# Performance work log

Measured on AMD Instinct MI355X. Metric: run time of the kernel, lower is better.

The kernel has to match this reference:

```python
import jax, jax.numpy as jnp
import numpy as np

NU, NI, E = 50000, 20000, 400000
IN, HID, OUT = 128, 256, 128
NEG_SLOPE_ATTN = 0.2   # DGL GATConv default
NEG_SLOPE_ACT = 0.01   # F.leaky_relu default
BN_EPS = 1e-5


def setup_inputs() -> dict:
    key = jax.random.key(0)
    ks = jax.random.split(key, 32)
    d = {}
    d["x_user"] = jax.random.normal(ks[0], (NU, IN), jnp.float32)
    d["x_item"] = jax.random.normal(ks[1], (NI, IN), jnp.float32)
    d["eu"] = jax.random.randint(ks[2], (E,), 0, NU, jnp.int32)
    d["ei"] = jax.random.randint(ks[3], (E,), 0, NI, jnp.int32)
    i = 4
    dims = [(IN, 4, 64), (HID, 4, 64), (HID, 4, 64), (HID, 4, 32)]
    for L, (fin, H, dh) in enumerate(dims):
        for rel in ("ui", "iu"):
            d[f"W{L}_{rel}"] = jax.random.normal(ks[i], (fin, H * dh), jnp.float32) * 0.1; i += 1
            d[f"A{L}_{rel}"] = jax.random.normal(ks[i], (2, H, dh), jnp.float32) * 0.1; i += 1
    # BN params: [layer, (gamma,beta), HID]; gamma near 1, beta near 0
    gu = 1.0 + 0.05 * jax.random.normal(ks[i], (3, 1, HID), jnp.float32); i += 1
    bu = 0.05 * jax.random.normal(ks[i], (3, 1, HID), jnp.float32); i += 1
    gi = 1.0 + 0.05 * jax.random.normal(ks[i], (3, 1, HID), jnp.float32); i += 1
    bi = 0.05 * jax.random.normal(ks[i], (3, 1, HID), jnp.float32); i += 1
    d["bn_u"] = jnp.concatenate([gu, bu], axis=1)
    d["bn_i"] = jnp.concatenate([gi, bi], axis=1)
    return d


def _gat(x_src, x_dst, W, A, src, dst, n_dst):
    # Single-relation bipartite GATConv (DGL semantics).
    H, dh = A.shape[1], A.shape[2]
    hs = (x_src @ W).reshape(-1, H, dh)           # [Ns,H,dh]
    hd = (x_dst @ W).reshape(-1, H, dh)           # [Nd,H,dh]
    el = jnp.einsum('nhd,hd->nh', hs, A[0])
    er = jnp.einsum('nhd,hd->nh', hd, A[1])
    e = jax.nn.leaky_relu(el[src] + er[dst], NEG_SLOPE_ATTN)   # [E,H]
    emax = jax.ops.segment_max(e, dst, num_segments=n_dst)
    ee = jnp.exp(e - emax[dst])
    denom = jax.ops.segment_sum(ee, dst, num_segments=n_dst)
    alpha = ee / denom[dst]                       # segment softmax over in-edges
    out = jax.ops.segment_sum(hs[src] * alpha[..., None], dst, num_segments=n_dst)
    return out.reshape(n_dst, H * dh)


def _bn(x, gamma, beta):
    mu = x.mean(axis=0)
    var = x.var(axis=0)   # biased, matches torch BN normalization
    return gamma * (x - mu) * jax.lax.rsqrt(var + BN_EPS) + beta


def reference(x_user, x_item, eu, ei, W0_ui, W0_iu, A0_ui, A0_iu,
              W1_ui, W1_iu, A1_ui, A1_iu, W2_ui, W2_iu, A2_ui, A2_iu,
              W3_ui, W3_iu, A3_ui, A3_iu, bn_u, bn_i):
    Wui = [W0_ui, W1_ui, W2_ui]; Aui = [A0_ui, A1_ui, A2_ui]
    Wiu = [W0_iu, W1_iu, W2_iu]; Aiu = [A0_iu, A1_iu, A2_iu]
    hu, hi = x_user, x_item
    for L in range(3):
        ni = _gat(hu, hi, Wui[L], Aui[L], eu, ei, NI)   # user -> item
        nu = _gat(hi, hu, Wiu[L], Aiu[L], ei, eu, NU)   # item -> user
        nu = _bn(nu, bn_u[L, 0], bn_u[L, 1])
        ni = _bn(ni, bn_i[L, 0], bn_i[L, 1])
        if L == 2:   # last hidden layer uses tanh in non-residual path
            hu, hi = jnp.tanh(nu), jnp.tanh(ni)
        else:
            hu = jax.nn.leaky_relu(nu, NEG_SLOPE_ACT)
            hi = jax.nn.leaky_relu(ni, NEG_SLOPE_ACT)
    out_i = _gat(hu, hi, W3_ui, A3_ui, eu, ei, NI)
    out_u = _gat(hi, hu, W3_iu, A3_iu, ei, eu, NU)
    return jnp.concatenate([out_u, out_i], axis=0)   # [NU+NI, OUT]
```

## Files before the change

kernel.cpp:

```cpp
#include <hip/hip_runtime.h>

#define NUSERS 50000
#define NITEMS 20000
#define NEDGES 400000

typedef _Float16 f16;
typedef __attribute__((ext_vector_type(8))) _Float16 f16x8;
typedef __attribute__((ext_vector_type(4))) _Float16 f16x4;
typedef __attribute__((ext_vector_type(2))) _Float16 f16x2;
typedef __attribute__((ext_vector_type(4))) float f32x4;

__global__ void prep_k(const float* __restrict__ Wa, const float* __restrict__ Aa,
                       f16* __restrict__ Bta, float* __restrict__ efa,
                       const float* __restrict__ Wb, const float* __restrict__ Ab,
                       f16* __restrict__ Btb, float* __restrict__ efb,
                       int K, int Nw, int dh) {
  int t = blockIdx.x * blockDim.x + threadIdx.x;
  int half = K * Nw;
  if (t >= 2 * half) return;
  const float* W = (t < half) ? Wa : Wb;
  const float* A = (t < half) ? Aa : Ab;
  f16* Bt = (t < half) ? Bta : Btb;
  float* ef = (t < half) ? efa : efb;
  int t2 = (t < half) ? t : t - half;
  int n = t2 / K, k = t2 - n * K;
  Bt[t2] = (f16)W[(long)k * Nw + n];
  if (t2 < K * 8) {
    int j = t2 / (K * 4);
    int r = t2 - j * K * 4;
    int h = r / K, f = r - h * K;
    const float* Aj = A + j * Nw;
    float s = 0.f;
    for (int d = 0; d < dh; ++d) s += W[f * Nw + h * dh + d] * Aj[h * dh + d];
    ef[j * 4 * K + h * K + f] = s;
  }
}

__global__ void xcvt_k(const float* __restrict__ xu, f16* __restrict__ yu, long nu,
                       const float* __restrict__ xi, f16* __restrict__ yi, long ni) {
  long i = (long)blockIdx.x * blockDim.x + threadIdx.x;
  if (i < nu) yu[i] = (f16)xu[i];
  else if (i < nu + ni) yi[i - nu] = (f16)xi[i - nu];
}

__global__ __launch_bounds__(256) void hgemm2_k(const f16* __restrict__ Aa, const f16* __restrict__ Bta,
                                                f16* __restrict__ Ca, int Ma, int gya,
                                                const f16* __restrict__ Ab, const f16* __restrict__ Btb,
                                                f16* __restrict__ Cb, int Mb,
                                                int N, int K) {
  __shared__ f16 As[128 * 32];
  __shared__ f16 Bs[128 * 32];
  int by = blockIdx.y;
  const f16* A; const f16* Bt; f16* C; int M; int row0;
  if (by < gya) { A = Aa; Bt = Bta; C = Ca; M = Ma; row0 = by * 128; }
  else          { A = Ab; Bt = Btb; C = Cb; M = Mb; row0 = (by - gya) * 128; }
  int tid = threadIdx.x;
  int col0 = blockIdx.x * 128;
  int lane = tid & 63, wv = tid >> 6;
  int wr = (wv & 1) * 64, wc = (wv >> 1) * 64;
  int l16 = lane & 15, q = lane >> 4;
  f32x4 acc[4][4] = {};
  int r = tid >> 2, c8 = (tid & 3) * 8;
  for (int k0 = 0; k0 < K; k0 += 32) {
    int ra = min(row0 + r, M - 1);
    uint4 va = *(const uint4*)&A[(long)ra * K + k0 + c8];
    int ra2 = min(row0 + r + 64, M - 1);
    uint4 va2 = *(const uint4*)&A[(long)ra2 * K + k0 + c8];
    uint4 vb = *(const uint4*)&Bt[(long)(col0 + r) * K + k0 + c8];
    uint4 vb2 = *(const uint4*)&Bt[(long)(col0 + r + 64) * K + k0 + c8];
    *(uint4*)&As[r * 32 + c8] = va;
    *(uint4*)&As[(r + 64) * 32 + c8] = va2;
    *(uint4*)&Bs[r * 32 + c8] = vb;
    *(uint4*)&Bs[(r + 64) * 32 + c8] = vb2;
    __syncthreads();
    f16x8 af[4], bfr[4];
#pragma unroll
    for (int i = 0; i < 4; ++i) {
      af[i] = *(const f16x8*)&As[(wr + i * 16 + l16) * 32 + q * 8];
      bfr[i] = *(const f16x8*)&Bs[(wc + i * 16 + l16) * 32 + q * 8];
    }
#pragma unroll
    for (int i = 0; i < 4; ++i)
#pragma unroll
      for (int j = 0; j < 4; ++j)
        acc[i][j] = __builtin_amdgcn_mfma_f32_16x16x32_f16(af[i], bfr[j], acc[i][j], 0, 0, 0);
    __syncthreads();
  }
#pragma unroll
  for (int i = 0; i < 4; ++i) {
#pragma unroll
    for (int reg = 0; reg < 4; ++reg) {
      int rr = row0 + wr + i * 16 + q * 4 + reg;
      if (rr < M) {
#pragma unroll
        for (int j = 0; j < 4; ++j)
          C[(long)rr * N + col0 + wc + j * 16 + l16] = (f16)acc[i][j][reg];
      }
    }
  }
}

__global__ __launch_bounds__(256) void eler_k(
    const f16* __restrict__ hbu, const float* __restrict__ ef_ui, const float* __restrict__ ef_iu,
    float* __restrict__ el_u, float* __restrict__ er_u,
    const f16* __restrict__ hbi, float* __restrict__ el_i, float* __restrict__ er_i, int K) {
  __shared__ float xs[256];
  int b = blockIdx.x, t = threadIdx.x;
  const f16* hb; const float* elf; const float* erf; float* el; float* er; int n;
  if (b < NUSERS) { hb = hbu; elf = ef_ui; erf = ef_iu + 4 * K; el = el_u; er = er_u; n = b; }
  else            { hb = hbi; elf = ef_iu; erf = ef_ui + 4 * K; el = el_i; er = er_i; n = b - NUSERS; }
  if (t < K) xs[t] = (float)hb[(long)n * K + t];
  __syncthreads();
  int j = t >> 5, l = t & 31;
  const float* fr = (j < 4) ? (elf + j * K) : (erf + (j - 4) * K);
  float p = 0.f;
  for (int f = l; f < K; f += 32) p += xs[f] * fr[f];
#pragma unroll
  for (int off = 16; off; off >>= 1) p += __shfl_down(p, off, 32);
  if (l == 0) { if (j < 4) el[n * 4 + j] = p; else er[n * 4 + (j - 4)] = p; }
}

__global__ void hist_k(const int* __restrict__ ei, int* __restrict__ degi,
                       const int* __restrict__ eu, int* __restrict__ degu) {
  int e = blockIdx.x * blockDim.x + threadIdx.x;
  if (e < NEDGES) atomicAdd(&degi[ei[e]], 1);
  else if (e < 2 * NEDGES) atomicAdd(&degu[eu[e - NEDGES]], 1);
}

__global__ __launch_bounds__(256) void scan1_k(const int* __restrict__ deg,
                                               int* __restrict__ bsum, int N) {
  __shared__ int red[256];
  int base = blockIdx.x * 1024, t = threadIdx.x;
  int s = 0;
#pragma unroll
  for (int j = 0; j < 4; ++j) { int i = base + t * 4 + j; s += (i < N) ? deg[i] : 0; }
  red[t] = s; __syncthreads();
  for (int off = 128; off; off >>= 1) { if (t < off) red[t] += red[t + off]; __syncthreads(); }
  if (t == 0) bsum[blockIdx.x] = red[0];
}

__global__ void scan2_k(int* __restrict__ bsum, int nb) {
  if (threadIdx.x == 0) {
    int run = 0;
    for (int i = 0; i < nb; ++i) { int v = bsum[i]; bsum[i] = run; run += v; }
  }
}

__global__ __launch_bounds__(256) void scan3_k(const int* __restrict__ deg,
                                               const int* __restrict__ bsum,
                                               int* __restrict__ rowptr, int N) {
  __shared__ int tsum[256];
  int base = blockIdx.x * 1024, t = threadIdx.x;
  int v[4]; int s = 0;
#pragma unroll
  for (int j = 0; j < 4; ++j) { int i = base + t * 4 + j; v[j] = (i < N) ? deg[i] : 0; s += v[j]; }
  tsum[t] = s; __syncthreads();
  for (int off = 1; off < 256; off <<= 1) {
    int x = (t >= off) ? tsum[t - off] : 0;
    __syncthreads();
    tsum[t] += x;
    __syncthreads();
  }
  int run = bsum[blockIdx.x] + ((t > 0) ? tsum[t - 1] : 0);
#pragma unroll
  for (int j = 0; j < 4; ++j) {
    int i = base + t * 4 + j;
    if (i < N) rowptr[i] = run;
    run += v[j];
  }
}

__global__ void setval_k(int* __restrict__ p, int v) { *p = v; }

__global__ void copy2_k(const int* __restrict__ a, int* __restrict__ b, int Na,
                        const int* __restrict__ c, int* __restrict__ d, int Nc) {
  int i = blockIdx.x * blockDim.x + threadIdx.x;
  if (i < Na) b[i] = a[i];
  else if (i < Na + Nc) d[i - Na] = c[i - Na];
}

__global__ void scat_k(const int* __restrict__ ei, const int* __restrict__ eu,
                       int* __restrict__ curi, int* __restrict__ srci,
                       int* __restrict__ curu, int* __restrict__ srcu) {
  int e = blockIdx.x * blockDim.x + threadIdx.x;
  if (e < NEDGES) {
    int p = atomicAdd(&curi[ei[e]], 1);
    srci[p] = eu[e];
  } else if (e < 2 * NEDGES) {
    int e2 = e - NEDGES;
    int p = atomicAdd(&curu[eu[e2]], 1);
    srcu[p] = ei[e2];
  }
}

template <int W, int DH, typename OUT>
__global__ __launch_bounds__(256) void agg_k(
    const float* __restrict__ elA, const float* __restrict__ erA,
    const int* __restrict__ rpA, const int* __restrict__ srcA,
    const f16* __restrict__ hsA, OUT* __restrict__ outA, int nA,
    const float* __restrict__ elB, const float* __restrict__ erB,
    const int* __restrict__ rpB, const int* __restrict__ srcB,
    const f16* __restrict__ hsB, OUT* __restrict__ outB, int nB) {
  constexpr int CPL = W >> 6;
  constexpr int SHIFT = (W == 256) ? 9 : 8;
  constexpr bool OF16 = (sizeof(OUT) == 2);
  __shared__ float alds[4][256];
  __shared__ int soff[4][64];
  int wv = threadIdx.x >> 6;
  int g = blockIdx.x * 4 + wv;
  int lane = threadIdx.x & 63;
  const float* el; const float* er; const int* rp; const int* srcv;
  const f16* hs; OUT* outp; int d;
  if (g < nA)           { el = elA; er = erA; rp = rpA; srcv = srcA; hs = hsA; outp = outA; d = g; }
  else if (g < nA + nB) { el = elB; er = erB; rp = rpB; srcv = srcB; hs = hsB; outp = outB; d = g - nA; }
  else return;
  int s0 = rp[d], s1 = rp[d + 1];
  int deg = s1 - s0;
  int c0 = lane * CPL;
  int h = c0 / DH;
  long obase = (long)d * W + c0;
  if (deg == 0) {
#pragma unroll
    for (int q = 0; q < CPL; ++q) outp[obase + q] = (OUT)0.f;
    return;
  }
  const float NEG = -3.0e38f;
  float acc[CPL];
#pragma unroll
  for (int q = 0; q < CPL; ++q) acc[q] = 0.f;
  float inv;

  if (deg <= 64) {
    int hh = lane & 3, p = lane >> 2;
    float er_h = er[d * 4 + hh];
    float vv[4];
    float vmax = NEG;
#pragma unroll
    for (int j = 0; j < 4; ++j) {
      int slot = j * 16 + p;
      vv[j] = NEG;
      if (slot < deg) {
        int sj = srcv[s0 + slot];
        if (hh == 0) soff[wv][slot] = sj << SHIFT;
        float v = el[sj * 4 + hh] + er_h;
        v = v > 0.f ? v : 0.2f * v;
        vv[j] = v;
        vmax = fmaxf(vmax, v);
      }
    }
#pragma unroll
    for (int off = 4; off < 64; off <<= 1) vmax = fmaxf(vmax, __shfl_xor(vmax, off, 64));
    float ssum = 0.f;
#pragma unroll
    for (int j = 0; j < 4; ++j) {
      int slot = j * 16 + p;
      if (slot < deg) {
        float e = expf(vv[j] - vmax);
        alds[wv][slot * 4 + hh] = e;
        ssum += e;
      } else {
        alds[wv][slot * 4 + hh] = 0.f;
        if (hh == 0) soff[wv][slot] = 0;
      }
    }
#pragma unroll
    for (int off = 4; off < 64; off <<= 1) ssum += __shfl_xor(ssum, off, 64);
    float Sh = __shfl(ssum, (lane & ~3) | h, 64);
    inv = 1.0f / Sh;
    const char* hbase = (const char*)hs + (size_t)c0 * sizeof(f16);
    int degp = (deg + 3) & ~3;
    for (int j = 0; j < degp; j += 4) {
      float aj[4]; int oj[4];
#pragma unroll
      for (int u = 0; u < 4; ++u) {
        aj[u] = alds[wv][(j + u) * 4 + h];
        oj[u] = soff[wv][j + u];
      }
      if constexpr (CPL == 4) {
        f16x4 vj[4];
#pragma unroll
        for (int u = 0; u < 4; ++u)
          vj[u] = *(const f16x4*)(hbase + (size_t)(unsigned)oj[u]);
#pragma unroll
        for (int u = 0; u < 4; ++u) {
          acc[0] += aj[u] * (float)vj[u][0];
          acc[1] += aj[u] * (float)vj[u][1];
          acc[2] += aj[u] * (float)vj[u][2];
          acc[3] += aj[u] * (float)vj[u][3];
        }
      } else {
        f16x2 vj[4];
#pragma unroll
        for (int u = 0; u < 4; ++u)
          vj[u] = *(const f16x2*)(hbase + (size_t)(unsigned)oj[u]);
#pragma unroll
        for (int u = 0; u < 4; ++u) {
          acc[0] += aj[u] * (float)vj[u][0];
          acc[1] += aj[u] * (float)vj[u][1];
        }
      }
    }
  } else {
    float4 er4 = *(const float4*)&er[d * 4];
    float m0 = NEG, m1 = NEG, m2 = NEG, m3 = NEG;
    for (int k = s0 + lane; k < s1; k += 64) {
      int s = srcv[k];
      float4 e4 = *(const float4*)&el[s * 4];
      float v;
      v = e4.x + er4.x; v = v > 0.f ? v : 0.2f * v; m0 = fmaxf(m0, v);
      v = e4.y + er4.y; v = v > 0.f ? v : 0.2f * v; m1 = fmaxf(m1, v);
      v = e4.z + er4.z; v = v > 0.f ? v : 0.2f * v; m2 = fmaxf(m2, v);
      v = e4.w + er4.w; v = v > 0.f ? v : 0.2f * v; m3 = fmaxf(m3, v);
    }
#pragma unroll
    for (int off = 32; off; off >>= 1) {
      m0 = fmaxf(m0, __shfl_xor(m0, off, 64));
      m1 = fmaxf(m1, __shfl_xor(m1, off, 64));
      m2 = fmaxf(m2, __shfl_xor(m2, off, 64));
      m3 = fmaxf(m3, __shfl_xor(m3, off, 64));
    }
    float S0 = 0.f, S1 = 0.f, S2 = 0.f, S3 = 0.f;
    for (int k = s0 + lane; k < s1; k += 64) {
      int s = srcv[k];
      float4 e4 = *(const float4*)&el[s * 4];
      float v;
      v = e4.x + er4.x; v = v > 0.f ? v : 0.2f * v; S0 += expf(v - m0);
      v = e4.y + er4.y; v = v > 0.f ? v : 0.2f * v; S1 += expf(v - m1);
      v = e4.z + er4.z; v = v > 0.f ? v : 0.2f * v; S2 += expf(v - m2);
      v = e4.w + er4.w; v = v > 0.f ? v : 0.2f * v; S3 += expf(v - m3);
    }
#pragma unroll
    for (int off = 32; off; off >>= 1) {
      S0 += __shfl_xor(S0, off, 64);
      S1 += __shfl_xor(S1, off, 64);
      S2 += __shfl_xor(S2, off, 64);
      S3 += __shfl_xor(S3, off, 64);
    }
    float mh = h == 0 ? m0 : h == 1 ? m1 : h == 2 ? m2 : m3;
    float Sh = h == 0 ? S0 : h == 1 ? S1 : h == 2 ? S2 : S3;
    float erh = h == 0 ? er4.x : h == 1 ? er4.y : h == 2 ? er4.z : er4.w;
    inv = 1.0f / Sh;
    for (int k = s0; k < s1; ++k) {
      int s = srcv[k];
      float v = el[s * 4 + h] + erh; v = v > 0.f ? v : 0.2f * v;
      float a = expf(v - mh);
      const f16* row = &hs[(long)s * W + c0];
      if constexpr (CPL == 4) {
        f16x4 hv = *(const f16x4*)row;
        acc[0] += a * (float)hv[0]; acc[1] += a * (float)hv[1];
        acc[2] += a * (float)hv[2]; acc[3] += a * (float)hv[3];
      } else {
        f16x2 hv = *(const f16x2*)row;
        acc[0] += a * (float)hv[0]; acc[1] += a * (float)hv[1];
      }
    }
  }
  if constexpr (OF16) {
    if constexpr (CPL == 4) {
      f16x4 o = { (f16)(acc[0] * inv), (f16)(acc[1] * inv), (f16)(acc[2] * inv), (f16)(acc[3] * inv) };
      *(f16x4*)&outp[obase] = o;
    } else {
      f16x2 o = { (f16)(acc[0] * inv), (f16)(acc[1] * inv) };
      *(f16x2*)&outp[obase] = o;
    }
  } else {
    if constexpr (CPL == 4) {
      *(float4*)&outp[obase] = make_float4(acc[0] * inv, acc[1] * inv, acc[2] * inv, acc[3] * inv);
    } else {
      *(float2*)&outp[obase] = make_float2(acc[0] * inv, acc[1] * inv);
    }
  }
}

__global__ void zero2_k(float* __restrict__ a, float* __restrict__ b) {
  int t = threadIdx.x;
  a[t] = 0.f; b[t] = 0.f;
}

__global__ __launch_bounds__(256) void bn_stats2_k(const f16* __restrict__ xu, float* __restrict__ su, int Nu, int gU,
                                                   const f16* __restrict__ xi, float* __restrict__ si, int Ni) {
  const int C = 256;
  int b = blockIdx.x;
  const f16* x; float* sums; int N; int r0;
  if (b < gU) { x = xu; sums = su; N = Nu; r0 = b * 64; }
  else        { x = xi; sums = si; N = Ni; r0 = (b - gU) * 64; }
  int c = threadIdx.x;
  int r1 = min(r0 + 64, N);
  float s = 0.f, s2 = 0.f;
  for (int r = r0; r < r1; ++r) {
    float v = (float)x[(long)r * C + c];
    s += v; s2 += v * v;
  }
  atomicAdd(&sums[c], s);
  atomicAdd(&sums[C + c], s2);
}

__global__ __launch_bounds__(256) void bn_fused_k(
    const f16* __restrict__ xu, const float* __restrict__ su, const float* __restrict__ gbu,
    f16* __restrict__ yu, int Nu,
    const f16* __restrict__ xi, const float* __restrict__ si, const float* __restrict__ gbi,
    f16* __restrict__ yi, int Ni,
    const float* __restrict__ efu, const float* __restrict__ efiu,
    float* __restrict__ el_u, float* __restrict__ er_u,
    float* __restrict__ el_i, float* __restrict__ er_i, int act) {
  const int Kn = 256;
  __shared__ float xs[256];
  int b = blockIdx.x, t = threadIdx.x;
  const f16* x; const float* sums; const float* gb; f16* y; int n; int N;
  const float* elf; const float* erf; float* el; float* er;
  if (b < Nu) { x = xu; sums = su; gb = gbu; y = yu; n = b; N = Nu; elf = efu;  erf = efiu + 4 * Kn; el = el_u; er = er_u; }
  else        { x = xi; sums = si; gb = gbi; y = yi; n = b - Nu; N = Ni; elf = efiu; erf = efu + 4 * Kn;  el = el_i; er = er_i; }
  long base = (long)n * 256;
  float val = (float)x[base + t];
  float inv_n = 1.0f / (float)N;
  float mean = sums[t] * inv_n;
  float var = sums[256 + t] * inv_n - mean * mean;
  float v = gb[t] * (val - mean) * rsqrtf(var + 1e-5f) + gb[256 + t];
  v = act ? tanhf(v) : (v > 0.f ? v : 0.01f * v);
  y[base + t] = (f16)v;
  xs[t] = v;
  __syncthreads();
  int j = t >> 5, l = t & 31;
  const float* fr = (j < 4) ? (elf + j * Kn) : (erf + (j - 4) * Kn);
  float p = 0.f;
  for (int f = l; f < Kn; f += 32) p += xs[f] * fr[f];
#pragma unroll
  for (int off = 16; off; off >>= 1) p += __shfl_down(p, off, 32);
  if (l == 0) { if (j < 4) el[n * 4 + j] = p; else er[n * 4 + (j - 4)] = p; }
}

extern "C" void kernel_launch(void* const* d_in, const int* in_sizes, int n_in,
                              void* d_out, int out_size, void* d_ws, size_t ws_size,
                              hipStream_t stream) {
  const float* x_user = (const float*)d_in[0];
  const float* x_item = (const float*)d_in[1];
  const int* eu = (const int*)d_in[2];
  const int* ei = (const int*)d_in[3];
  const float *Wm[4][2], *Am[4][2];
  for (int L = 0; L < 4; ++L) {
    Wm[L][0] = (const float*)d_in[4 + L * 4 + 0];
    Am[L][0] = (const float*)d_in[4 + L * 4 + 1];
    Wm[L][1] = (const float*)d_in[4 + L * 4 + 2];
    Am[L][1] = (const float*)d_in[4 + L * 4 + 3];
  }
  const float* bnu = (const float*)d_in[20];
  const float* bni = (const float*)d_in[21];
  float* out = (float*)d_out;

  float* ws = (float*)d_ws;
  size_t o = 0;
  float* el_u = ws + o; o += (size_t)NUSERS * 4;
  float* er_u = ws + o; o += (size_t)NUSERS * 4;
  float* el_i = ws + o; o += (size_t)NITEMS * 4;
  float* er_i = ws + o; o += (size_t)NITEMS * 4;
  float* ef_all[4][2];
  for (int L = 0; L < 4; ++L)
    for (int rl = 0; rl < 2; ++rl) { ef_all[L][rl] = ws + o; o += 2048; }
  float* bns_u = ws + o; o += 512;
  float* bns_i = ws + o; o += 512;
  f16* hb_u   = (f16*)(ws + o); o += (size_t)NUSERS * 128;
  f16* hb_i   = (f16*)(ws + o); o += (size_t)NITEMS * 128;
  f16* hsb_u  = (f16*)(ws + o); o += (size_t)NUSERS * 128;
  f16* hsb_i  = (f16*)(ws + o); o += (size_t)NITEMS * 128;
  f16* aggh_u = (f16*)(ws + o); o += (size_t)NUSERS * 128;
  f16* aggh_i = (f16*)(ws + o); o += (size_t)NITEMS * 128;
  f16* Bt_all[4][2];
  for (int L = 0; L < 4; ++L) {
    int K = (L == 0) ? 128 : 256;
    int W = (L == 3) ? 128 : 256;
    for (int rl = 0; rl < 2; ++rl) { Bt_all[L][rl] = (f16*)(ws + o); o += (size_t)K * W / 2; }
  }
  int* deg_i    = (int*)(ws + o); o += NITEMS;
  int* deg_u    = (int*)(ws + o); o += NUSERS;
  int* rowptr_i = (int*)(ws + o); o += NITEMS + 1;
  int* rowptr_u = (int*)(ws + o); o += NUSERS + 1;
  int* cur_i    = (int*)(ws + o); o += NITEMS;
  int* cur_u    = (int*)(ws + o); o += NUSERS;
  int* bsum     = (int*)(ws + o); o += 256;
  int* csrsrc_i = (int*)(ws + o); o += NEDGES;
  int* csrsrc_u = (int*)(ws + o); o += NEDGES;

  const int gE2 = (2 * NEDGES + 255) / 256;
  const int nb_i = (NITEMS + 1023) / 1024;
  const int nb_u = (NUSERS + 1023) / 1024;
  const int gU = (NUSERS + 63) / 64;
  const int gI = (NITEMS + 63) / 64;

  hipMemsetAsync(deg_i, 0, (NITEMS + NUSERS) * sizeof(int), stream);
  hist_k<<<dim3(gE2), dim3(256), 0, stream>>>(ei, deg_i, eu, deg_u);
  scan1_k<<<dim3(nb_i), dim3(256), 0, stream>>>(deg_i, bsum, NITEMS);
  scan2_k<<<dim3(1), dim3(64), 0, stream>>>(bsum, nb_i);
  scan3_k<<<dim3(nb_i), dim3(256), 0, stream>>>(deg_i, bsum, rowptr_i, NITEMS);
  setval_k<<<dim3(1), dim3(1), 0, stream>>>(rowptr_i + NITEMS, NEDGES);
  scan1_k<<<dim3(nb_u), dim3(256), 0, stream>>>(deg_u, bsum, NUSERS);
  scan2_k<<<dim3(1), dim3(64), 0, stream>>>(bsum, nb_u);
  scan3_k<<<dim3(nb_u), dim3(256), 0, stream>>>(deg_u, bsum, rowptr_u, NUSERS);
  setval_k<<<dim3(1), dim3(1), 0, stream>>>(rowptr_u + NUSERS, NEDGES);
  copy2_k<<<dim3((NITEMS + NUSERS + 255) / 256), dim3(256), 0, stream>>>(rowptr_i, cur_i, NITEMS, rowptr_u, cur_u, NUSERS);
  scat_k<<<dim3(gE2), dim3(256), 0, stream>>>(ei, eu, cur_i, csrsrc_i, cur_u, csrsrc_u);

  for (int L = 0; L < 4; ++L) {
    int K = (L == 0) ? 128 : 256;
    int dh = (L == 3) ? 32 : 64;
    int W = 4 * dh;
    prep_k<<<dim3((2 * K * W + 255) / 256), dim3(256), 0, stream>>>(
        Wm[L][0], Am[L][0], Bt_all[L][0], ef_all[L][0],
        Wm[L][1], Am[L][1], Bt_all[L][1], ef_all[L][1], K, W, dh);
  }

  xcvt_k<<<dim3(((NUSERS + NITEMS) * 128 + 255) / 256), dim3(256), 0, stream>>>(
      x_user, hb_u, (long)NUSERS * 128, x_item, hb_i, (long)NITEMS * 128);
  eler_k<<<dim3(NUSERS + NITEMS), dim3(256), 0, stream>>>(
      hb_u, ef_all[0][0], ef_all[0][1], el_u, er_u, hb_i, el_i, er_i, 128);

  int K = 128;
  for (int L = 0; L < 4; ++L) {
    const int dh = (L == 3) ? 32 : 64;
    const int W = 4 * dh;

    const int gya = (NUSERS + 127) / 128, gyb = (NITEMS + 127) / 128;
    hgemm2_k<<<dim3(W / 128, gya + gyb), dim3(256), 0, stream>>>(
        hb_u, Bt_all[L][0], hsb_u, NUSERS, gya, hb_i, Bt_all[L][1], hsb_i, NITEMS, W, K);

    const int gAgg = (NITEMS + NUSERS + 3) / 4;
    if (L < 3) {
      agg_k<256, 64, f16><<<dim3(gAgg), dim3(256), 0, stream>>>(
          el_u, er_i, rowptr_i, csrsrc_i, hsb_u, aggh_i, NITEMS,
          el_i, er_u, rowptr_u, csrsrc_u, hsb_i, aggh_u, NUSERS);
      zero2_k<<<dim3(1), dim3(512), 0, stream>>>(bns_u, bns_i);
      bn_stats2_k<<<dim3(gU + gI), dim3(256), 0, stream>>>(aggh_u, bns_u, NUSERS, gU, aggh_i, bns_i, NITEMS);
      bn_fused_k<<<dim3(NUSERS + NITEMS), dim3(256), 0, stream>>>(
          aggh_u, bns_u, bnu + L * 512, hb_u, NUSERS,
          aggh_i, bns_i, bni + L * 512, hb_i, NITEMS,
          ef_all[L + 1][0], ef_all[L + 1][1],
          el_u, er_u, el_i, er_i, L == 2);
      K = 256;
    } else {
      agg_k<128, 32, float><<<dim3(gAgg), dim3(256), 0, stream>>>(
          el_u, er_i, rowptr_i, csrsrc_i, hsb_u, out + (size_t)NUSERS * 128, NITEMS,
          el_i, er_u, rowptr_u, csrsrc_u, hsb_i, out, NUSERS);
    }
  }
}
```

Measured before the change: 910.0 us.

## Fuse input conversion into eler, tile weight transpose, drop tiny kernels

Folds the fp32-to-fp16 input conversion into the el/er projection kernel, so x is read once instead of being converted and then re-read. Replaces the strided per-element weight transpose with an LDS-tiled transpose. Removes the setval and per-layer zero kernels by folding the rowptr end write into scan2 and zeroing all BN stat buffers with the initial memset. Marks aggregation output stores as nontemporal. Together these aim to cut launch count and redundant memory traffic, with the risk that nontemporal stores hurt when the next kernel reads the aggregation output straight back.

After: 908.6 us. Within noise of the previous version (-0.1%).

```diff
diff --git a/kernel.cpp b/kernel.cpp
--- a/kernel.cpp
+++ b/kernel.cpp
@@ -9,23 +9,44 @@
 typedef __attribute__((ext_vector_type(4))) _Float16 f16x4;
 typedef __attribute__((ext_vector_type(2))) _Float16 f16x2;
 typedef __attribute__((ext_vector_type(4))) float f32x4;
-
-__global__ void prep_k(const float* __restrict__ Wa, const float* __restrict__ Aa,
-                       f16* __restrict__ Bta, float* __restrict__ efa,
-                       const float* __restrict__ Wb, const float* __restrict__ Ab,
-                       f16* __restrict__ Btb, float* __restrict__ efb,
-                       int K, int Nw, int dh) {
-  int t = blockIdx.x * blockDim.x + threadIdx.x;
-  int half = K * Nw;
-  if (t >= 2 * half) return;
-  const float* W = (t < half) ? Wa : Wb;
-  const float* A = (t < half) ? Aa : Ab;
-  f16* Bt = (t < half) ? Bta : Btb;
-  float* ef = (t < half) ? efa : efb;
-  int t2 = (t < half) ? t : t - half;
-  int n = t2 / K, k = t2 - n * K;
-  Bt[t2] = (f16)W[(long)k * Nw + n];
-  if (t2 < K * 8) {
+typedef __attribute__((ext_vector_type(2))) float f32x2;
+
+__global__ __launch_bounds__(256) void prep2_k(
+    const float* __restrict__ Wa, const float* __restrict__ Aa,
+    f16* __restrict__ Bta, float* __restrict__ efa,
+    const float* __restrict__ Wb, const float* __restrict__ Ab,
+    f16* __restrict__ Btb, float* __restrict__ efb,
+    int K, int Nw, int dh) {
+  __shared__ float lds[32][33];
+  int ntile = (K >> 5) * (Nw >> 5);
+  int b = blockIdx.x, t = threadIdx.x;
+  if (b < 2 * ntile) {
+    const float* W = (b < ntile) ? Wa : Wb;
+    f16* Bt = (b < ntile) ? Bta : Btb;
+    int tt = (b < ntile) ? b : b - ntile;
+    int ntc = Nw >> 5;
+    int tr = tt / ntc, tc = tt - tr * ntc;
+    int tx = t & 31, ty = t >> 5;
+#pragma unroll
+    for (int p = 0; p < 4; ++p) {
+      int k = tr * 32 + ty + p * 8;
+      int n = tc * 32 + tx;
+      lds[ty + p * 8][tx] = W[(long)k * Nw + n];
+    }
+    __syncthreads();
+#pragma unroll
+    for (int p = 0; p < 4; ++p) {
+      int n = tc * 32 + ty + p * 8;
+      int k = tr * 32 + tx;
+      Bt[(long)n * K + k] = (f16)lds[tx][ty + p * 8];
+    }
+  } else {
+    int idx = (b - 2 * ntile) * 256 + t;
+    if (idx >= 2 * K * 8) return;
+    const float* W = (idx < K * 8) ? Wa : Wb;
+    const float* A = (idx < K * 8) ? Aa : Ab;
+    float* ef = (idx < K * 8) ? efa : efb;
+    int t2 = (idx < K * 8) ? idx : idx - K * 8;
     int j = t2 / (K * 4);
     int r = t2 - j * K * 4;
     int h = r / K, f = r - h * K;
@@ -34,13 +55,6 @@
     for (int d = 0; d < dh; ++d) s += W[f * Nw + h * dh + d] * Aj[h * dh + d];
     ef[j * 4 * K + h * K + f] = s;
   }
-}
-
-__global__ void xcvt_k(const float* __restrict__ xu, f16* __restrict__ yu, long nu,
-                       const float* __restrict__ xi, f16* __restrict__ yi, long ni) {
-  long i = (long)blockIdx.x * blockDim.x + threadIdx.x;
-  if (i < nu) yu[i] = (f16)xu[i];
-  else if (i < nu + ni) yi[i - nu] = (f16)xi[i - nu];
 }
 
 __global__ __launch_bounds__(256) void hgemm2_k(const f16* __restrict__ Aa, const f16* __restrict__ Bta,
@@ -100,16 +114,22 @@
   }
 }
 
-__global__ __launch_bounds__(256) void eler_k(
-    const f16* __restrict__ hbu, const float* __restrict__ ef_ui, const float* __restrict__ ef_iu,
+__global__ __launch_bounds__(256) void eler2_k(
+    const float* __restrict__ xu, f16* __restrict__ hbu,
+    const float* __restrict__ ef_ui, const float* __restrict__ ef_iu,
     float* __restrict__ el_u, float* __restrict__ er_u,
-    const f16* __restrict__ hbi, float* __restrict__ el_i, float* __restrict__ er_i, int K) {
+    const float* __restrict__ xi, f16* __restrict__ hbi,
+    float* __restrict__ el_i, float* __restrict__ er_i, int K) {
   __shared__ float xs[256];
   int b = blockIdx.x, t = threadIdx.x;
-  const f16* hb; const float* elf; const float* erf; float* el; float* er; int n;
-  if (b < NUSERS) { hb = hbu; elf = ef_ui; erf = ef_iu + 4 * K; el = el_u; er = er_u; n = b; }
-  else            { hb = hbi; elf = ef_iu; erf = ef_ui + 4 * K; el = el_i; er = er_i; n = b - NUSERS; }
-  if (t < K) xs[t] = (float)hb[(long)n * K + t];
+  const float* x; f16* hb; const float* elf; const float* erf; float* el; float* er; int n;
+  if (b < NUSERS) { x = xu; hb = hbu; elf = ef_ui; erf = ef_iu + 4 * K; el = el_u; er = er_u; n = b; }
+  else            { x = xi; hb = hbi; elf = ef_iu; erf = ef_ui + 4 * K; el = el_i; er = er_i; n = b - NUSERS; }
+  if (t < K) {
+    float v = x[(long)n * K + t];
+    hb[(long)n * K + t] = (f16)v;
+    xs[t] = v;
+  }
   __syncthreads();
   int j = t >> 5, l = t & 31;
   const float* fr = (j < 4) ? (elf + j * K) : (erf + (j - 4) * K);
@@ -139,10 +159,11 @@
   if (t == 0) bsum[blockIdx.x] = red[0];
 }
 
-__global__ void scan2_k(int* __restrict__ bsum, int nb) {
+__global__ void scan2_k(int* __restrict__ bsum, int nb, int* __restrict__ endp, int endv) {
   if (threadIdx.x == 0) {
     int run = 0;
     for (int i = 0; i < nb; ++i) { int v = bsum[i]; bsum[i] = run; run += v; }
+    *endp = endv;
   }
 }
 
@@ -169,8 +190,6 @@
     run += v[j];
   }
 }
-
-__global__ void setval_k(int* __restrict__ p, int v) { *p = v; }
 
 __global__ void copy2_k(const int* __restrict__ a, int* __restrict__ b, int Na,
                         const int* __restrict__ c, int* __restrict__ d, int Nc) {
@@ -358,23 +377,20 @@
   if constexpr (OF16) {
     if constexpr (CPL == 4) {
       f16x4 o = { (f16)(acc[0] * inv), (f16)(acc[1] * inv), (f16)(acc[2] * inv), (f16)(acc[3] * inv) };
-      *(f16x4*)&outp[obase] = o;
+      __builtin_nontemporal_store(o, (f16x4*)&outp[obase]);
     } else {
       f16x2 o = { (f16)(acc[0] * inv), (f16)(acc[1] * inv) };
-      *(f16x2*)&outp[obase] = o;
+      __builtin_nontemporal_store(o, (f16x2*)&outp[obase]);
     }
   } else {
     if constexpr (CPL == 4) {
-      *(float4*)&outp[obase] = make_float4(acc[0] * inv, acc[1] * inv, acc[2] * inv, acc[3] * inv);
+      f32x4 o = { acc[0] * inv, acc[1] * inv, acc[2] * inv, acc[3] * inv };
+      __builtin_nontemporal_store(o, (f32x4*)&outp[obase]);
     } else {
-      *(float2*)&outp[obase] = make_float2(acc[0] * inv, acc[1] * inv);
-    }
-  }
-}
-
-__global__ void zero2_k(float* __restrict__ a, float* __restrict__ b) {
-  int t = threadIdx.x;
-  a[t] = 0.f; b[t] = 0.f;
+      f32x2 o = { acc[0] * inv, acc[1] * inv };
+      __builtin_nontemporal_store(o, (f32x2*)&outp[obase]);
+    }
+  }
 }
 
 __global__ __launch_bounds__(256) void bn_stats2_k(const f16* __restrict__ xu, float* __restrict__ su, int Nu, int gU,
@@ -456,8 +472,6 @@
   float* ef_all[4][2];
   for (int L = 0; L < 4; ++L)
     for (int rl = 0; rl < 2; ++rl) { ef_all[L][rl] = ws + o; o += 2048; }
-  float* bns_u = ws + o; o += 512;
-  float* bns_i = ws + o; o += 512;
   f16* hb_u   = (f16*)(ws + o); o += (size_t)NUSERS * 128;
   f16* hb_i   = (f16*)(ws + o); o += (size_t)NITEMS * 128;
   f16* hsb_u  = (f16*)(ws + o); o += (size_t)NUSERS * 128;
@@ -470,15 +484,16 @@
     int W = (L == 3) ? 128 : 256;
     for (int rl = 0; rl < 2; ++rl) { Bt_all[L][rl] = (f16*)(ws + o); o += (size_t)K * W / 2; }
   }
+  float* bns_all = ws + o; o += 3 * 1024;
   int* deg_i    = (int*)(ws + o); o += NITEMS;
   int* deg_u    = (int*)(ws + o); o += NUSERS;
-  int* rowptr_i = (int*)(ws + o); o += NITEMS + 1;
-  int* rowptr_u = (int*)(ws + o); o += NUSERS + 1;
+  int* rowptr_i = (int*)(ws + o); o += NITEMS + 4;
+  int* rowptr_u = (int*)(ws + o); o += NUSERS + 4;
   int* cur_i    = (int*)(ws + o); o += NITEMS;
   int* cur_u    = (int*)(ws + o); o += NUSERS;
   int* bsum     = (int*)(ws + o); o += 256;
-  int* csrsrc_i = (int*)(ws + o); o += NEDGES;
-  int* csrsrc_u = (int*)(ws + o); o += NEDGES;
+  int* csrsrc_i = (int*)(ws + o); o += NEDGES + 4;
+  int* csrsrc_u = (int*)(ws + o); o += NEDGES + 4;
 
   const int gE2 = (2 * NEDGES + 255) / 256;
   const int nb_i = (NITEMS + 1023) / 1024;
@@ -486,16 +501,14 @@
   const int gU = (NUSERS + 63) / 64;
   const int gI = (NITEMS + 63) / 64;
 
-  hipMemsetAsync(deg_i, 0, (NITEMS + NUSERS) * sizeof(int), stream);
+  hipMemsetAsync(bns_all, 0, (3 * 1024 + NITEMS + NUSERS) * sizeof(float), stream);
   hist_k<<<dim3(gE2), dim3(256), 0, stream>>>(ei, deg_i, eu, deg_u);
   scan1_k<<<dim3(nb_i), dim3(256), 0, stream>>>(deg_i, bsum, NITEMS);
-  scan2_k<<<dim3(1), dim3(64), 0, stream>>>(bsum, nb_i);
+  scan2_k<<<dim3(1), dim3(64), 0, stream>>>(bsum, nb_i, rowptr_i + NITEMS, NEDGES);
   scan3_k<<<dim3(nb_i), dim3(256), 0, stream>>>(deg_i, bsum, rowptr_i, NITEMS);
-  setval_k<<<dim3(1), dim3(1), 0, stream>>>(rowptr_i + NITEMS, NEDGES);
   scan1_k<<<dim3(nb_u), dim3(256), 0, stream>>>(deg_u, bsum, NUSERS);
-  scan2_k<<<dim3(1), dim3(64), 0, stream>>>(bsum, nb_u);
+  scan2_k<<<dim3(1), dim3(64), 0, stream>>>(bsum, nb_u, rowptr_u + NUSERS, NEDGES);
   scan3_k<<<dim3(nb_u), dim3(256), 0, stream>>>(deg_u, bsum, rowptr_u, NUSERS);
-  setval_k<<<dim3(1), dim3(1), 0, stream>>>(rowptr_u + NUSERS, NEDGES);
   copy2_k<<<dim3((NITEMS + NUSERS + 255) / 256), dim3(256), 0, stream>>>(rowptr_i, cur_i, NITEMS, rowptr_u, cur_u, NUSERS);
   scat_k<<<dim3(gE2), dim3(256), 0, stream>>>(ei, eu, cur_i, csrsrc_i, cur_u, csrsrc_u);
 
@@ -503,35 +516,37 @@
     int K = (L == 0) ? 128 : 256;
     int dh = (L == 3) ? 32 : 64;
     int W = 4 * dh;
-    prep_k<<<dim3((2 * K * W + 255) / 256), dim3(256), 0, stream>>>(
+    int ntile2 = 2 * (K / 32) * (W / 32);
+    int gef = (2 * K * 8 + 255) / 256;
+    prep2_k<<<dim3(ntile2 + gef), dim3(256), 0, stream>>>(
         Wm[L][0], Am[L][0], Bt_all[L][0], ef_all[L][0],
         Wm[L][1], Am[L][1], Bt_all[L][1], ef_all[L][1], K, W, dh);
   }
 
-  xcvt_k<<<dim3(((NUSERS + NITEMS) * 128 + 255) / 256), dim3(256), 0, stream>>>(
-      x_user, hb_u, (long)NUSERS * 128, x_item, hb_i, (long)NITEMS * 128);
-  eler_k<<<dim3(NUSERS + NITEMS), dim3(256), 0, stream>>>(
-      hb_u, ef_all[0][0], ef_all[0][1], el_u, er_u, hb_i, el_i, er_i, 128);
+  eler2_k<<<dim3(NUSERS + NITEMS), dim3(256), 0, stream>>>(
+      x_user, hb_u, ef_all[0][0], ef_all[0][1], el_u, er_u,
+      x_item, hb_i, el_i, er_i, 128);
 
   int K = 128;
+  const int gAgg = (NITEMS + NUSERS + 3) / 4;
+  const int gya = (NUSERS + 127) / 128, gyb = (NITEMS + 127) / 128;
   for (int L = 0; L < 4; ++L) {
     const int dh = (L == 3) ? 32 : 64;
     const int W = 4 * dh;
 
-    const int gya = (NUSERS + 127) / 128, gyb = (NITEMS + 127) / 128;
     hgemm2_k<<<dim3(W / 128, gya + gyb), dim3(256), 0, stream>>>(
         hb_u, Bt_all[L][0], hsb_u, NUSERS, gya, hb_i, Bt_all[L][1], hsb_i, NITEMS, W, K);
 
-    const int gAgg = (NITEMS + NUSERS + 3) / 4;
     if (L < 3) {
+      float* su = bns_all + (size_t)L * 1024;
+      float* si = su + 512;
       agg_k<256, 64, f16><<<dim3(gAgg), dim3(256), 0, stream>>>(
           el_u, er_i, rowptr_i, csrsrc_i, hsb_u, aggh_i, NITEMS,
           el_i, er_u, rowptr_u, csrsrc_u, hsb_i, aggh_u, NUSERS);
-      zero2_k<<<dim3(1), dim3(512), 0, stream>>>(bns_u, bns_i);
-      bn_stats2_k<<<dim3(gU + gI), dim3(256), 0, stream>>>(aggh_u, bns_u, NUSERS, gU, aggh_i, bns_i, NITEMS);
+      bn_stats2_k<<<dim3(gU + gI), dim3(256), 0, stream>>>(aggh_u, su, NUSERS, gU, aggh_i, si, NITEMS);
       bn_fused_k<<<dim3(NUSERS + NITEMS), dim3(256), 0, stream>>>(
-          aggh_u, bns_u, bnu + L * 512, hb_u, NUSERS,
-          aggh_i, bns_i, bni + L * 512, hb_i, NITEMS,
+          aggh_u, su, bnu + L * 512, hb_u, NUSERS,
+          aggh_i, si, bni + L * 512, hb_i, NITEMS,
           ef_all[L + 1][0], ef_all[L + 1][1],
           el_u, er_u, el_i, er_i, L == 2);
       K = 256;
```
